# Kernel tuning notes

Hardware: AMD Instinct MI355X
Metric: run time of the kernel (lower is better)

## Reference

```python
import jax, jax.numpy as jnp
import numpy as np

N_NODES = 50000

def _sage(x, src, dst, Wl, bl, Wr):
    # PyG SAGEConv(aggr='mean'): out = lin_l(mean_{j in N(i)} x_j) + lin_r(x_i)
    msg = x[src]                                                    # [E, F] gather
    agg = jax.ops.segment_sum(msg, dst, num_segments=N_NODES)      # [N, F]
    cnt = jax.ops.segment_sum(jnp.ones((src.shape[0],), x.dtype), dst, num_segments=N_NODES)
    agg = agg / jnp.maximum(cnt, 1.0)[:, None]                     # mean aggregate
    return agg @ Wl + bl + x @ Wr                                   # lin_l has bias, lin_r does not


def setup_inputs() -> dict:
    key = jax.random.key(0)
    ks = jax.random.split(key, 14)
    d_in, d_h, d_out, n_edges = 128, 64, 4, 800000
    s = lambda k, shp, fan: jax.random.normal(k, shp, jnp.float32) * (1.0 / np.sqrt(fan))
    return {
        'x': jax.random.normal(ks[0], (N_NODES, d_in), jnp.float32),
        'edge_index': jax.random.randint(ks[1], (2, n_edges), 0, N_NODES, jnp.int64),
        'Wl1': s(ks[2], (d_in, d_h), d_in), 'bl1': jnp.zeros((d_h,), jnp.float32),
        'Wr1': s(ks[3], (d_in, d_h), d_in),
        'Wl2': s(ks[4], (d_h, d_h), d_h), 'bl2': jnp.zeros((d_h,), jnp.float32),
        'Wr2': s(ks[5], (d_h, d_h), d_h),
        'Wl3': s(ks[6], (d_h, d_h), d_h), 'bl3': jnp.zeros((d_h,), jnp.float32),
        'Wr3': s(ks[7], (d_h, d_h), d_h),
        'Wp': s(ks[8], (2 * d_h, d_out), 2 * d_h), 'bp': jnp.zeros((d_out,), jnp.float32),
    }


def reference(x, edge_index, Wl1, bl1, Wr1, Wl2, bl2, Wr2, Wl3, bl3, Wr3, Wp, bp):
    src, dst = edge_index[0], edge_index[1]
    # dropout is identity in eval mode
    h = jax.nn.elu(_sage(x, src, dst, Wl1, bl1, Wr1))
    h = jax.nn.elu(_sage(h, src, dst, Wl2, bl2, Wr2))
    h = jax.nn.elu(_sage(h, src, dst, Wl3, bl3, Wr3))
    edge_feat = jnp.concatenate([h[src], h[dst]], axis=1)  # [E, 2*hidden]
    return edge_feat @ Wp + bp                              # [E, output_dim]
```

## Files before the change

kernel.cpp:

```cpp
#include <hip/hip_runtime.h>
#include <hip/hip_bf16.h>

#define N_NODES 50000
#define N_EDGES 800000
#define D_IN 128
#define D_H 64
#define SCAN_BLOCKS 196
#define HIST_BLOCKS 3125
#define LIN1_BLOCKS 782
#define GL_BLOCKS 3125
#define ZROW 65535

#define F1L 0
#define F1R 8192
#define F2L 16384
#define F2R 20480
#define F3L 24576
#define F3R 28672
#define FRAG_TOTAL 32768

typedef short bf16x8 __attribute__((ext_vector_type(8)));
typedef float f32x4 __attribute__((ext_vector_type(4)));

__device__ __forceinline__ ushort f2bf(float f) {
    __hip_bfloat16 b = __float2bfloat16(f);
    return *reinterpret_cast<ushort*>(&b);
}
__device__ __forceinline__ float bf16_lo(unsigned int u) { return __uint_as_float(u << 16); }
__device__ __forceinline__ float bf16_hi(unsigned int u) { return __uint_as_float(u & 0xffff0000u); }

__device__ __forceinline__ void build_frag_one(const float* __restrict__ W, int local,
                                               ushort* __restrict__ frag, int fid) {
    int lane = local & 63;
    int ktnt = local >> 6;
    int kt = ktnt >> 2, nt = ktnt & 3;
    int quad = lane >> 4, col = lane & 15;
    ushort t0 = f2bf(W[(kt * 32 + quad * 8 + 0) * D_H + nt * 16 + col]);
    ushort t1 = f2bf(W[(kt * 32 + quad * 8 + 1) * D_H + nt * 16 + col]);
    ushort t2 = f2bf(W[(kt * 32 + quad * 8 + 2) * D_H + nt * 16 + col]);
    ushort t3 = f2bf(W[(kt * 32 + quad * 8 + 3) * D_H + nt * 16 + col]);
    ushort t4 = f2bf(W[(kt * 32 + quad * 8 + 4) * D_H + nt * 16 + col]);
    ushort t5 = f2bf(W[(kt * 32 + quad * 8 + 5) * D_H + nt * 16 + col]);
    ushort t6 = f2bf(W[(kt * 32 + quad * 8 + 6) * D_H + nt * 16 + col]);
    ushort t7 = f2bf(W[(kt * 32 + quad * 8 + 7) * D_H + nt * 16 + col]);
    uint4 v;
    v.x = (unsigned int)t0 | ((unsigned int)t1 << 16);
    v.y = (unsigned int)t2 | ((unsigned int)t3 << 16);
    v.z = (unsigned int)t4 | ((unsigned int)t5 << 16);
    v.w = (unsigned int)t6 | ((unsigned int)t7 << 16);
    *reinterpret_cast<uint4*>(frag + (size_t)fid * 8) = v;
}

__global__ void hist_frags_kernel(const int* __restrict__ dstv, int* __restrict__ cnt,
                                  ushort* __restrict__ rank,
                                  const float* __restrict__ Wl1, const float* __restrict__ Wr1,
                                  const float* __restrict__ Wl2, const float* __restrict__ Wr2,
                                  const float* __restrict__ Wl3, const float* __restrict__ Wr3,
                                  ushort* __restrict__ frag,
                                  ushort* __restrict__ Y1, ushort* __restrict__ Y2) {
    if (blockIdx.x < HIST_BLOCKS) {
        int e = blockIdx.x * 256 + threadIdx.x;
        if (e < N_EDGES) {
            int r = atomicAdd(&cnt[dstv[e]], 1);
            rank[e] = (ushort)r;
        }
    } else if (blockIdx.x < HIST_BLOCKS + 16) {
        int fid = (blockIdx.x - HIST_BLOCKS) * 256 + threadIdx.x;
        const float* W; int base;
        if (fid < 1024)      { W = Wl1; base = 0; }
        else if (fid < 2048) { W = Wr1; base = 1024; }
        else if (fid < 2560) { W = Wl2; base = 2048; }
        else if (fid < 3072) { W = Wr2; base = 2560; }
        else if (fid < 3584) { W = Wl3; base = 3072; }
        else                 { W = Wr3; base = 3584; }
        build_frag_one(W, fid - base, frag, fid);
    } else {
        int t = threadIdx.x;
        if (t < 64)       Y1[(size_t)ZROW * D_H + t] = 0;
        else if (t < 128) Y2[(size_t)ZROW * D_H + (t - 64)] = 0;
    }
}

__global__ void scan_partial(const int* __restrict__ cnt, int* __restrict__ blockSums) {
    __shared__ int s[256];
    int i = blockIdx.x * 256 + threadIdx.x;
    s[threadIdx.x] = (i < N_NODES) ? cnt[i] : 0;
    __syncthreads();
    for (int off = 128; off > 0; off >>= 1) {
        if (threadIdx.x < off) s[threadIdx.x] += s[threadIdx.x + off];
        __syncthreads();
    }
    if (threadIdx.x == 0) blockSums[blockIdx.x] = s[0];
}

__global__ void scan_final(const int* __restrict__ cnt, const int* __restrict__ blockSums,
                           int* __restrict__ row_ptr) {
    __shared__ int s[256];
    __shared__ int bs[256];
    int t = threadIdx.x;
    bs[t] = (t < SCAN_BLOCKS) ? blockSums[t] : 0;
    int i = blockIdx.x * 256 + t;
    s[t] = (i < N_NODES) ? cnt[i] : 0;
    __syncthreads();
    for (int off = 1; off < 256; off <<= 1) {
        int tmp1 = (t >= off) ? s[t - off] : 0;
        int tmp2 = (t >= off) ? bs[t - off] : 0;
        __syncthreads();
        s[t] += tmp1;
        bs[t] += tmp2;
        __syncthreads();
    }
    int blockExcl = (blockIdx.x > 0) ? bs[blockIdx.x - 1] : 0;
    int excl = blockExcl + ((t > 0) ? s[t - 1] : 0);
    if (i < N_NODES) row_ptr[i] = excl;
    if (i == 0) row_ptr[N_NODES] = N_EDGES;
}

__device__ __forceinline__ void lin1_body(int gwave, int lane, const float* __restrict__ hin,
                                          const ushort* __restrict__ fragWl,
                                          const ushort* __restrict__ fragWr,
                                          ushort* __restrict__ Y, ushort* __restrict__ Zb) {
    constexpr int KT = D_IN / 32;
    int m0 = gwave * 16;
    if (m0 >= N_NODES) return;
    int col = lane & 15;
    int quad = lane >> 4;

    bf16x8 blf2[KT][4], brf[KT][4];
#pragma unroll
    for (int kt = 0; kt < KT; ++kt)
#pragma unroll
        for (int nt = 0; nt < 4; ++nt) {
            size_t off = (size_t)((kt * 4 + nt) * 64 + lane) * 8;
            blf2[kt][nt] = __builtin_bit_cast(bf16x8, *reinterpret_cast<const uint4*>(fragWl + off));
            brf[kt][nt] = __builtin_bit_cast(bf16x8, *reinterpret_cast<const uint4*>(fragWr + off));
        }

    f32x4 accl0 = {0.f,0.f,0.f,0.f}, accl1 = accl0, accl2 = accl0, accl3 = accl0;
    f32x4 accr0 = accl0, accr1 = accl0, accr2 = accl0, accr3 = accl0;
    const float* arow = hin + (size_t)(m0 + col) * D_IN + quad * 8;
#pragma unroll
    for (int kt = 0; kt < KT; ++kt) {
        float4 a_lo = *reinterpret_cast<const float4*>(arow + kt * 32);
        float4 a_hi = *reinterpret_cast<const float4*>(arow + kt * 32 + 4);
        bf16x8 a;
        a[0] = (short)f2bf(a_lo.x); a[1] = (short)f2bf(a_lo.y);
        a[2] = (short)f2bf(a_lo.z); a[3] = (short)f2bf(a_lo.w);
        a[4] = (short)f2bf(a_hi.x); a[5] = (short)f2bf(a_hi.y);
        a[6] = (short)f2bf(a_hi.z); a[7] = (short)f2bf(a_hi.w);
        accl0 = __builtin_amdgcn_mfma_f32_16x16x32_bf16(a, blf2[kt][0], accl0, 0, 0, 0);
        accl1 = __builtin_amdgcn_mfma_f32_16x16x32_bf16(a, blf2[kt][1], accl1, 0, 0, 0);
        accl2 = __builtin_amdgcn_mfma_f32_16x16x32_bf16(a, blf2[kt][2], accl2, 0, 0, 0);
        accl3 = __builtin_amdgcn_mfma_f32_16x16x32_bf16(a, blf2[kt][3], accl3, 0, 0, 0);
        accr0 = __builtin_amdgcn_mfma_f32_16x16x32_bf16(a, brf[kt][0], accr0, 0, 0, 0);
        accr1 = __builtin_amdgcn_mfma_f32_16x16x32_bf16(a, brf[kt][1], accr1, 0, 0, 0);
        accr2 = __builtin_amdgcn_mfma_f32_16x16x32_bf16(a, brf[kt][2], accr2, 0, 0, 0);
        accr3 = __builtin_amdgcn_mfma_f32_16x16x32_bf16(a, brf[kt][3], accr3, 0, 0, 0);
    }
#pragma unroll
    for (int reg = 0; reg < 4; ++reg) {
        size_t r = (size_t)(m0 + quad * 4 + reg) * D_H;
        ushort* yp = Y + r;
        yp[0 * 16 + col] = f2bf(accl0[reg]);
        yp[1 * 16 + col] = f2bf(accl1[reg]);
        yp[2 * 16 + col] = f2bf(accl2[reg]);
        yp[3 * 16 + col] = f2bf(accl3[reg]);
        ushort* zp = Zb + r;
        zp[0 * 16 + col] = f2bf(accr0[reg]);
        zp[1 * 16 + col] = f2bf(accr1[reg]);
        zp[2 * 16 + col] = f2bf(accr2[reg]);
        zp[3 * 16 + col] = f2bf(accr3[reg]);
    }
}

__global__ void lin1_fill_kernel(const float* __restrict__ x, const ushort* __restrict__ wfrag,
                                 const int* __restrict__ srcv, const int* __restrict__ dstv,
                                 const ushort* __restrict__ rank, const int* __restrict__ row_ptr,
                                 ushort* __restrict__ csr_src,
                                 ushort* __restrict__ Y, ushort* __restrict__ Zb) {
    if (blockIdx.x < LIN1_BLOCKS) {
        int gwave = (blockIdx.x * 256 + threadIdx.x) >> 6;
        lin1_body(gwave, threadIdx.x & 63, x, wfrag + F1L, wfrag + F1R, Y, Zb);
    } else {
        int e = (blockIdx.x - LIN1_BLOCKS) * 256 + threadIdx.x;
        if (e < N_EDGES) {
            int d = dstv[e];
            int pos = row_ptr[d] + (int)rank[e];
            csr_src[pos] = (ushort)srcv[e];
        }
    }
}

template <bool FUSE_PROJ>
__global__ void gather_lin_kernel(const ushort* __restrict__ Y, const ushort* __restrict__ Zb,
                                  const float* __restrict__ bl,
                                  const int* __restrict__ row_ptr, const ushort* __restrict__ csr_src,
                                  const ushort* __restrict__ fragWl, const ushort* __restrict__ fragWr,
                                  ushort* __restrict__ Ynext, ushort* __restrict__ Zbnext,
                                  const float* __restrict__ Wp,
                                  float* __restrict__ ps, float* __restrict__ pd) {
    __shared__ ushort Hs[16][72];
    int w = threadIdx.x >> 6;
    int lane = threadIdx.x & 63;
    int wv = (blockIdx.x << 2) + w;
    int n0 = wv << 2;
    int g = lane >> 4;
    int l = lane & 15;

    int rp[5];
#pragma unroll
    for (int i = 0; i < 5; ++i) rp[i] = row_ptr[n0 + i];
    int deg[4];
#pragma unroll
    for (int n = 0; n < 4; ++n) deg[n] = rp[n + 1] - rp[n];
    int maxdeg = deg[0];
#pragma unroll
    for (int n = 1; n < 4; ++n) maxdeg = deg[n] > maxdeg ? deg[n] : maxdeg;

    float acc[4][4] = {{0.f}};
    const uint2* __restrict__ Y2 = reinterpret_cast<const uint2*>(Y);

    for (int base = 0; base < maxdeg; base += 64) {
        int idxv[4];
#pragma unroll
        for (int n = 0; n < 4; ++n) {
            int t = (int)csr_src[rp[n] + base + lane];
            idxv[n] = (base + lane < deg[n]) ? t : ZROW;
        }
        int kmax = maxdeg - base; if (kmax > 64) kmax = 64;
        for (int k = 0; k < kmax; k += 16) {
            uint2 rr[4][4];
#pragma unroll
            for (int n = 0; n < 4; ++n)
#pragma unroll
                for (int j = 0; j < 4; ++j) {
                    int s = __shfl(idxv[n], k + 4 * j + g);
                    rr[n][j] = Y2[s * 16 + l];
                }
#pragma unroll
            for (int n = 0; n < 4; ++n)
#pragma unroll
                for (int j = 0; j < 4; ++j) {
                    acc[n][0] += bf16_lo(rr[n][j].x); acc[n][1] += bf16_hi(rr[n][j].x);
                    acc[n][2] += bf16_lo(rr[n][j].y); acc[n][3] += bf16_hi(rr[n][j].y);
                }
        }
    }

#pragma unroll
    for (int n = 0; n < 4; ++n)
#pragma unroll
        for (int f = 0; f < 4; ++f) {
            acc[n][f] += __shfl_xor(acc[n][f], 16);
            acc[n][f] += __shfl_xor(acc[n][f], 32);
        }

    int node = n0 + g;
    float dgf = (g == 0) ? (float)deg[0] : (g == 1) ? (float)deg[1]
              : (g == 2) ? (float)deg[2] : (float)deg[3];
    float c0 = (g == 0) ? acc[0][0] : (g == 1) ? acc[1][0] : (g == 2) ? acc[2][0] : acc[3][0];
    float c1 = (g == 0) ? acc[0][1] : (g == 1) ? acc[1][1] : (g == 2) ? acc[2][1] : acc[3][1];
    float c2 = (g == 0) ? acc[0][2] : (g == 1) ? acc[1][2] : (g == 2) ? acc[2][2] : acc[3][2];
    float c3 = (g == 0) ? acc[0][3] : (g == 1) ? acc[1][3] : (g == 2) ? acc[2][3] : acc[3][3];
    float inv = 1.0f / fmaxf(dgf, 1.0f);
    float4 bv = reinterpret_cast<const float4*>(bl)[l];
    uint2 zr = reinterpret_cast<const uint2*>(Zb)[node * 16 + l];
    float v0 = c0 * inv + bv.x + bf16_lo(zr.x);
    float v1 = c1 * inv + bv.y + bf16_hi(zr.x);
    float v2 = c2 * inv + bv.z + bf16_lo(zr.y);
    float v3 = c3 * inv + bv.w + bf16_hi(zr.y);
    float o0 = v0 > 0.f ? v0 : expm1f(v0);
    float o1 = v1 > 0.f ? v1 : expm1f(v1);
    float o2 = v2 > 0.f ? v2 : expm1f(v2);
    float o3 = v3 > 0.f ? v3 : expm1f(v3);

    if constexpr (FUSE_PROJ) {
        float p0 = 0.f, p1 = 0.f, p2 = 0.f, p3 = 0.f;
        float q0 = 0.f, q1 = 0.f, q2 = 0.f, q3 = 0.f;
        float ov[4] = {o0, o1, o2, o3};
#pragma unroll
        for (int j = 0; j < 4; ++j) {
            int k = 4 * l + j;
            float4 wt = reinterpret_cast<const float4*>(Wp)[k];
            float4 wb = reinterpret_cast<const float4*>(Wp)[D_H + k];
            p0 += ov[j] * wt.x; p1 += ov[j] * wt.y; p2 += ov[j] * wt.z; p3 += ov[j] * wt.w;
            q0 += ov[j] * wb.x; q1 += ov[j] * wb.y; q2 += ov[j] * wb.z; q3 += ov[j] * wb.w;
        }
#pragma unroll
        for (int off = 1; off < 16; off <<= 1) {
            p0 += __shfl_xor(p0, off); p1 += __shfl_xor(p1, off);
            p2 += __shfl_xor(p2, off); p3 += __shfl_xor(p3, off);
            q0 += __shfl_xor(q0, off); q1 += __shfl_xor(q1, off);
            q2 += __shfl_xor(q2, off); q3 += __shfl_xor(q3, off);
        }
        if (l == 0) {
            float4 pv; pv.x = p0; pv.y = p1; pv.z = p2; pv.w = p3;
            float4 qv; qv.x = q0; qv.y = q1; qv.z = q2; qv.w = q3;
            reinterpret_cast<float4*>(ps)[node] = pv;
            reinterpret_cast<float4*>(pd)[node] = qv;
        }
    } else {
        ushort4 ob;
        ob.x = f2bf(o0); ob.y = f2bf(o1); ob.z = f2bf(o2); ob.w = f2bf(o3);
        int localrow = w * 4 + g;
        *reinterpret_cast<ushort4*>(&Hs[localrow][4 * l]) = ob;
        __syncthreads();

        int col = lane & 15;
        int quad = lane >> 4;
        bf16x8 blf0 = __builtin_bit_cast(bf16x8,
            *reinterpret_cast<const uint4*>(fragWl + (size_t)((0 * 4 + w) * 64 + lane) * 8));
        bf16x8 blf1 = __builtin_bit_cast(bf16x8,
            *reinterpret_cast<const uint4*>(fragWl + (size_t)((1 * 4 + w) * 64 + lane) * 8));
        bf16x8 brf0 = __builtin_bit_cast(bf16x8,
            *reinterpret_cast<const uint4*>(fragWr + (size_t)((0 * 4 + w) * 64 + lane) * 8));
        bf16x8 brf1 = __builtin_bit_cast(bf16x8,
            *reinterpret_cast<const uint4*>(fragWr + (size_t)((1 * 4 + w) * 64 + lane) * 8));
        bf16x8 a0 = __builtin_bit_cast(bf16x8,
            *reinterpret_cast<const uint4*>(&Hs[col][quad * 8]));
        bf16x8 a1 = __builtin_bit_cast(bf16x8,
            *reinterpret_cast<const uint4*>(&Hs[col][32 + quad * 8]));
        f32x4 accl = {0.f,0.f,0.f,0.f};
        f32x4 accr = {0.f,0.f,0.f,0.f};
        accl = __builtin_amdgcn_mfma_f32_16x16x32_bf16(a0, blf0, accl, 0, 0, 0);
        accl = __builtin_amdgcn_mfma_f32_16x16x32_bf16(a1, blf1, accl, 0, 0, 0);
        accr = __builtin_amdgcn_mfma_f32_16x16x32_bf16(a0, brf0, accr, 0, 0, 0);
        accr = __builtin_amdgcn_mfma_f32_16x16x32_bf16(a1, brf1, accr, 0, 0, 0);

        int n0base = blockIdx.x * 16;
#pragma unroll
        for (int reg = 0; reg < 4; ++reg) {
            size_t r = (size_t)(n0base + quad * 4 + reg) * D_H + w * 16 + col;
            Ynext[r]  = f2bf(accl[reg]);
            Zbnext[r] = f2bf(accr[reg]);
        }
    }
}

__global__ void edge_final_kernel(const int* __restrict__ srcv, const int* __restrict__ dstv,
                                  const float* __restrict__ ps, const float* __restrict__ pd,
                                  const float* __restrict__ bp, float* __restrict__ out) {
    int e = blockIdx.x * 256 + threadIdx.x;
    const int HALF = N_EDGES / 2;
    if (e >= HALF) return;
    int e2 = e + HALF;
    int s0 = srcv[e], d0 = dstv[e];
    int s1 = srcv[e2], d1 = dstv[e2];
    float4 a0 = reinterpret_cast<const float4*>(ps)[s0];
    float4 b0 = reinterpret_cast<const float4*>(pd)[d0];
    float4 a1 = reinterpret_cast<const float4*>(ps)[s1];
    float4 b1 = reinterpret_cast<const float4*>(pd)[d1];
    float bx = bp[0], by = bp[1], bz = bp[2], bw = bp[3];
    float4 o0, o1;
    o0.x = a0.x + b0.x + bx; o0.y = a0.y + b0.y + by;
    o0.z = a0.z + b0.z + bz; o0.w = a0.w + b0.w + bw;
    o1.x = a1.x + b1.x + bx; o1.y = a1.y + b1.y + by;
    o1.z = a1.z + b1.z + bz; o1.w = a1.w + b1.w + bw;
    reinterpret_cast<float4*>(out)[e] = o0;
    reinterpret_cast<float4*>(out)[e2] = o1;
}

extern "C" void kernel_launch(void* const* d_in, const int* in_sizes, int n_in,
                              void* d_out, int out_size, void* d_ws, size_t ws_size,
                              hipStream_t stream) {
    const float* x   = (const float*)d_in[0];
    const int*   ei  = (const int*)d_in[1];
    const float* Wl1 = (const float*)d_in[2];
    const float* bl1 = (const float*)d_in[3];
    const float* Wr1 = (const float*)d_in[4];
    const float* Wl2 = (const float*)d_in[5];
    const float* bl2 = (const float*)d_in[6];
    const float* Wr2 = (const float*)d_in[7];
    const float* Wl3 = (const float*)d_in[8];
    const float* bl3 = (const float*)d_in[9];
    const float* Wr3 = (const float*)d_in[10];
    const float* Wp  = (const float*)d_in[11];
    const float* bp  = (const float*)d_in[12];
    float* out = (float*)d_out;

    const int* srcv = ei;
    const int* dstv = ei + N_EDGES;

    int*   cnt       = (int*)d_ws;
    int*   blockSums = cnt + 50000;
    int*   row_ptr   = blockSums + 256;
    ushort* rank     = (ushort*)(row_ptr + 50001);
    ushort* csr_src  = rank + 800000;
    ushort* wfrag = (ushort*)(((uintptr_t)(csr_src + 800000 + 4096) + 127) & ~(uintptr_t)127);
    ushort* Y1  = (ushort*)(((uintptr_t)(wfrag + FRAG_TOTAL) + 127) & ~(uintptr_t)127);
    ushort* Y2  = Y1 + (size_t)65536 * D_H;
    ushort* Zb1 = Y2 + (size_t)65536 * D_H;
    ushort* Zb2 = Zb1 + (size_t)N_NODES * D_H;
    float* ps = (float*)(((uintptr_t)(Zb2 + (size_t)N_NODES * D_H) + 15) & ~(uintptr_t)15);
    float* pd = ps + (size_t)N_NODES * 4;

    hipMemsetAsync(cnt, 0, N_NODES * sizeof(int), stream);
    hist_frags_kernel<<<HIST_BLOCKS + 17, 256, 0, stream>>>(dstv, cnt, rank, Wl1, Wr1, Wl2, Wr2,
                                                            Wl3, Wr3, wfrag, Y1, Y2);
    scan_partial<<<SCAN_BLOCKS, 256, 0, stream>>>(cnt, blockSums);
    scan_final<<<SCAN_BLOCKS, 256, 0, stream>>>(cnt, blockSums, row_ptr);

    lin1_fill_kernel<<<LIN1_BLOCKS + HIST_BLOCKS, 256, 0, stream>>>(x, wfrag, srcv, dstv,
                                                                    rank, row_ptr, csr_src,
                                                                    Y1, Zb1);

    gather_lin_kernel<false><<<GL_BLOCKS, 256, 0, stream>>>(Y1, Zb1, bl1, row_ptr, csr_src,
                                                            wfrag + F2L, wfrag + F2R, Y2, Zb2,
                                                            nullptr, nullptr, nullptr);

    gather_lin_kernel<false><<<GL_BLOCKS, 256, 0, stream>>>(Y2, Zb2, bl2, row_ptr, csr_src,
                                                            wfrag + F3L, wfrag + F3R, Y1, Zb1,
                                                            nullptr, nullptr, nullptr);

    gather_lin_kernel<true><<<GL_BLOCKS, 256, 0, stream>>>(Y1, Zb1, bl3, row_ptr, csr_src,
                                                           nullptr, nullptr, nullptr, nullptr,
                                                           Wp, ps, pd);

    edge_final_kernel<<<(N_EDGES / 2 + 255) / 256, 256, 0, stream>>>(srcv, dstv, ps, pd, bp, out);
}
```

Measured before the change: 235.6 us.

## Sort nodes by degree into bins so gather waves get balanced neighbor counts

Builds a 64-bin degree histogram during the scan and a counting-sort permutation of nodes by degree. The gather/linear kernels then process nodes in permuted order, so the four nodes sharing a wave have similar degrees and less lane time is wasted waiting on the maximum degree. Output rows are scattered through a shared-memory node-id table. The edge output kernel also now handles four edges per thread instead of two. The cost is extra atomics, a perm array, and scattered row writes that lose contiguity.

```diff
diff --git a/kernel.cpp b/kernel.cpp
--- a/kernel.cpp
+++ b/kernel.cpp
@@ -8,8 +8,10 @@
 #define SCAN_BLOCKS 196
 #define HIST_BLOCKS 3125
 #define LIN1_BLOCKS 782
+#define PERM_BLOCKS 196
 #define GL_BLOCKS 3125
 #define ZROW 65535
+#define DBINS 64
 
 #define F1L 0
 #define F1R 8192
@@ -81,20 +83,28 @@
     }
 }
 
-__global__ void scan_partial(const int* __restrict__ cnt, int* __restrict__ blockSums) {
+__global__ void scan_partial(const int* __restrict__ cnt, int* __restrict__ blockSums,
+                             int* __restrict__ dhist) {
     __shared__ int s[256];
-    int i = blockIdx.x * 256 + threadIdx.x;
-    s[threadIdx.x] = (i < N_NODES) ? cnt[i] : 0;
+    __shared__ int ldh[DBINS];
+    int t = threadIdx.x;
+    if (t < DBINS) ldh[t] = 0;
+    int i = blockIdx.x * 256 + t;
+    int myc = (i < N_NODES) ? cnt[i] : 0;
+    s[t] = myc;
     __syncthreads();
+    if (i < N_NODES) atomicAdd(&ldh[myc < DBINS ? myc : DBINS - 1], 1);
     for (int off = 128; off > 0; off >>= 1) {
-        if (threadIdx.x < off) s[threadIdx.x] += s[threadIdx.x + off];
+        if (t < off) s[t] += s[t + off];
         __syncthreads();
     }
-    if (threadIdx.x == 0) blockSums[blockIdx.x] = s[0];
+    if (t == 0) blockSums[blockIdx.x] = s[0];
+    if (t < DBINS && ldh[t] > 0) atomicAdd(&dhist[t], ldh[t]);
 }
 
 __global__ void scan_final(const int* __restrict__ cnt, const int* __restrict__ blockSums,
-                           int* __restrict__ row_ptr) {
+                           int* __restrict__ row_ptr,
+                           const int* __restrict__ dhist, int* __restrict__ dcur) {
     __shared__ int s[256];
     __shared__ int bs[256];
     int t = threadIdx.x;
@@ -114,6 +124,17 @@
     int excl = blockExcl + ((t > 0) ? s[t - 1] : 0);
     if (i < N_NODES) row_ptr[i] = excl;
     if (i == 0) row_ptr[N_NODES] = N_EDGES;
+
+    if (blockIdx.x == 0 && t < DBINS) {
+        int c = dhist[t];
+        int v = c;
+#pragma unroll
+        for (int off = 1; off < DBINS; off <<= 1) {
+            int u = __shfl_up(v, off);
+            if (t >= off) v += u;
+        }
+        dcur[t] = v - c;
+    }
 }
 
 __device__ __forceinline__ void lin1_body(int gwave, int lane, const float* __restrict__ hin,
@@ -177,17 +198,27 @@
                                  const int* __restrict__ srcv, const int* __restrict__ dstv,
                                  const ushort* __restrict__ rank, const int* __restrict__ row_ptr,
                                  ushort* __restrict__ csr_src,
+                                 const int* __restrict__ cnt, int* __restrict__ dcur,
+                                 int* __restrict__ perm,
                                  ushort* __restrict__ Y, ushort* __restrict__ Zb) {
     if (blockIdx.x < LIN1_BLOCKS) {
         int gwave = (blockIdx.x * 256 + threadIdx.x) >> 6;
         lin1_body(gwave, threadIdx.x & 63, x, wfrag + F1L, wfrag + F1R, Y, Zb);
-    } else {
+    } else if (blockIdx.x < LIN1_BLOCKS + HIST_BLOCKS) {
         int e = (blockIdx.x - LIN1_BLOCKS) * 256 + threadIdx.x;
         if (e < N_EDGES) {
             int d = dstv[e];
             int pos = row_ptr[d] + (int)rank[e];
             csr_src[pos] = (ushort)srcv[e];
         }
+    } else {
+        int i = (blockIdx.x - LIN1_BLOCKS - HIST_BLOCKS) * 256 + threadIdx.x;
+        if (i < N_NODES) {
+            int deg = cnt[i];
+            int bin = deg < DBINS ? deg : DBINS - 1;
+            int pos = atomicAdd(&dcur[bin], 1);
+            perm[pos] = i;
+        }
     }
 }
 
@@ -195,24 +226,26 @@
 __global__ void gather_lin_kernel(const ushort* __restrict__ Y, const ushort* __restrict__ Zb,
                                   const float* __restrict__ bl,
                                   const int* __restrict__ row_ptr, const ushort* __restrict__ csr_src,
+                                  const int* __restrict__ perm,
                                   const ushort* __restrict__ fragWl, const ushort* __restrict__ fragWr,
                                   ushort* __restrict__ Ynext, ushort* __restrict__ Zbnext,
                                   const float* __restrict__ Wp,
                                   float* __restrict__ ps, float* __restrict__ pd) {
     __shared__ ushort Hs[16][72];
+    __shared__ int nid[16];
     int w = threadIdx.x >> 6;
     int lane = threadIdx.x & 63;
-    int wv = (blockIdx.x << 2) + w;
-    int n0 = wv << 2;
     int g = lane >> 4;
     int l = lane & 15;
-
-    int rp[5];
-#pragma unroll
-    for (int i = 0; i < 5; ++i) rp[i] = row_ptr[n0 + i];
-    int deg[4];
-#pragma unroll
-    for (int n = 0; n < 4; ++n) deg[n] = rp[n + 1] - rp[n];
+    int base16 = blockIdx.x * 16;
+
+    int nd[4], rpl[4], deg[4];
+#pragma unroll
+    for (int n = 0; n < 4; ++n) {
+        nd[n] = perm[base16 + w * 4 + n];
+        rpl[n] = row_ptr[nd[n]];
+        deg[n] = row_ptr[nd[n] + 1] - rpl[n];
+    }
     int maxdeg = deg[0];
 #pragma unroll
     for (int n = 1; n < 4; ++n) maxdeg = deg[n] > maxdeg ? deg[n] : maxdeg;
@@ -224,7 +257,7 @@
         int idxv[4];
 #pragma unroll
         for (int n = 0; n < 4; ++n) {
-            int t = (int)csr_src[rp[n] + base + lane];
+            int t = (int)csr_src[rpl[n] + base + lane];
             idxv[n] = (base + lane < deg[n]) ? t : ZROW;
         }
         int kmax = maxdeg - base; if (kmax > 64) kmax = 64;
@@ -255,7 +288,7 @@
             acc[n][f] += __shfl_xor(acc[n][f], 32);
         }
 
-    int node = n0 + g;
+    int node = (g == 0) ? nd[0] : (g == 1) ? nd[1] : (g == 2) ? nd[2] : nd[3];
     float dgf = (g == 0) ? (float)deg[0] : (g == 1) ? (float)deg[1]
               : (g == 2) ? (float)deg[2] : (float)deg[3];
     float c0 = (g == 0) ? acc[0][0] : (g == 1) ? acc[1][0] : (g == 2) ? acc[2][0] : acc[3][0];
@@ -303,6 +336,7 @@
         ushort4 ob;
         ob.x = f2bf(o0); ob.y = f2bf(o1); ob.z = f2bf(o2); ob.w = f2bf(o3);
         int localrow = w * 4 + g;
+        if (l == 0) nid[localrow] = node;
         *reinterpret_cast<ushort4*>(&Hs[localrow][4 * l]) = ob;
         __syncthreads();
 
@@ -327,10 +361,10 @@
         accr = __builtin_amdgcn_mfma_f32_16x16x32_bf16(a0, brf0, accr, 0, 0, 0);
         accr = __builtin_amdgcn_mfma_f32_16x16x32_bf16(a1, brf1, accr, 0, 0, 0);
 
-        int n0base = blockIdx.x * 16;
 #pragma unroll
         for (int reg = 0; reg < 4; ++reg) {
-            size_t r = (size_t)(n0base + quad * 4 + reg) * D_H + w * 16 + col;
+            int trow = nid[quad * 4 + reg];
+            size_t r = (size_t)trow * D_H + w * 16 + col;
             Ynext[r]  = f2bf(accl[reg]);
             Zbnext[r] = f2bf(accr[reg]);
         }
@@ -341,23 +375,19 @@
                                   const float* __restrict__ ps, const float* __restrict__ pd,
                                   const float* __restrict__ bp, float* __restrict__ out) {
     int e = blockIdx.x * 256 + threadIdx.x;
-    const int HALF = N_EDGES / 2;
-    if (e >= HALF) return;
-    int e2 = e + HALF;
-    int s0 = srcv[e], d0 = dstv[e];
-    int s1 = srcv[e2], d1 = dstv[e2];
-    float4 a0 = reinterpret_cast<const float4*>(ps)[s0];
-    float4 b0 = reinterpret_cast<const float4*>(pd)[d0];
-    float4 a1 = reinterpret_cast<const float4*>(ps)[s1];
-    float4 b1 = reinterpret_cast<const float4*>(pd)[d1];
+    const int Q = N_EDGES / 4;
+    if (e >= Q) return;
     float bx = bp[0], by = bp[1], bz = bp[2], bw = bp[3];
-    float4 o0, o1;
-    o0.x = a0.x + b0.x + bx; o0.y = a0.y + b0.y + by;
-    o0.z = a0.z + b0.z + bz; o0.w = a0.w + b0.w + bw;
-    o1.x = a1.x + b1.x + bx; o1.y = a1.y + b1.y + by;
-    o1.z = a1.z + b1.z + bz; o1.w = a1.w + b1.w + bw;
-    reinterpret_cast<float4*>(out)[e] = o0;
-    reinterpret_cast<float4*>(out)[e2] = o1;
+#pragma unroll
+    for (int h = 0; h < 4; ++h) {
+        int ee = e + h * Q;
+        float4 a = reinterpret_cast<const float4*>(ps)[srcv[ee]];
+        float4 b = reinterpret_cast<const float4*>(pd)[dstv[ee]];
+        float4 o;
+        o.x = a.x + b.x + bx; o.y = a.y + b.y + by;
+        o.z = a.z + b.z + bz; o.w = a.w + b.w + bw;
+        reinterpret_cast<float4*>(out)[ee] = o;
+    }
 }
 
 extern "C" void kernel_launch(void* const* d_in, const int* in_sizes, int n_in,
@@ -382,9 +412,12 @@
     const int* dstv = ei + N_EDGES;
 
     int*   cnt       = (int*)d_ws;
-    int*   blockSums = cnt + 50000;
+    int*   dhist     = cnt + 50000;
+    int*   dcur      = dhist + 64;
+    int*   blockSums = dcur + 64;
     int*   row_ptr   = blockSums + 256;
-    ushort* rank     = (ushort*)(row_ptr + 50001);
+    int*   perm      = row_ptr + 50001;
+    ushort* rank     = (ushort*)(perm + 50000);
     ushort* csr_src  = rank + 800000;
     ushort* wfrag = (ushort*)(((uintptr_t)(csr_src + 800000 + 4096) + 127) & ~(uintptr_t)127);
     ushort* Y1  = (ushort*)(((uintptr_t)(wfrag + FRAG_TOTAL) + 127) & ~(uintptr_t)127);
@@ -394,27 +427,26 @@
     float* ps = (float*)(((uintptr_t)(Zb2 + (size_t)N_NODES * D_H) + 15) & ~(uintptr_t)15);
     float* pd = ps + (size_t)N_NODES * 4;
 
-    hipMemsetAsync(cnt, 0, N_NODES * sizeof(int), stream);
+    hipMemsetAsync(cnt, 0, (50000 + 64) * sizeof(int), stream);
     hist_frags_kernel<<<HIST_BLOCKS + 17, 256, 0, stream>>>(dstv, cnt, rank, Wl1, Wr1, Wl2, Wr2,
                                                             Wl3, Wr3, wfrag, Y1, Y2);
-    scan_partial<<<SCAN_BLOCKS, 256, 0, stream>>>(cnt, blockSums);
-    scan_final<<<SCAN_BLOCKS, 256, 0, stream>>>(cnt, blockSums, row_ptr);
-
-    lin1_fill_kernel<<<LIN1_BLOCKS + HIST_BLOCKS, 256, 0, stream>>>(x, wfrag, srcv, dstv,
-                                                                    rank, row_ptr, csr_src,
-                                                                    Y1, Zb1);
-
-    gather_lin_kernel<false><<<GL_BLOCKS, 256, 0, stream>>>(Y1, Zb1, bl1, row_ptr, csr_src,
+    scan_partial<<<SCAN_BLOCKS, 256, 0, stream>>>(cnt, blockSums, dhist);
+    scan_final<<<SCAN_BLOCKS, 256, 0, stream>>>(cnt, blockSums, row_ptr, dhist, dcur);
+
+    lin1_fill_kernel<<<LIN1_BLOCKS + HIST_BLOCKS + PERM_BLOCKS, 256, 0, stream>>>(
+        x, wfrag, srcv, dstv, rank, row_ptr, csr_src, cnt, dcur, perm, Y1, Zb1);
+
+    gather_lin_kernel<false><<<GL_BLOCKS, 256, 0, stream>>>(Y1, Zb1, bl1, row_ptr, csr_src, perm,
                                                             wfrag + F2L, wfrag + F2R, Y2, Zb2,
                                                             nullptr, nullptr, nullptr);
 
-    gather_lin_kernel<false><<<GL_BLOCKS, 256, 0, stream>>>(Y2, Zb2, bl2, row_ptr, csr_src,
+    gather_lin_kernel<false><<<GL_BLOCKS, 256, 0, stream>>>(Y2, Zb2, bl2, row_ptr, csr_src, perm,
                                                             wfrag + F3L, wfrag + F3R, Y1, Zb1,
                                                             nullptr, nullptr, nullptr);
 
-    gather_lin_kernel<true><<<GL_BLOCKS, 256, 0, stream>>>(Y1, Zb1, bl3, row_ptr, csr_src,
+    gather_lin_kernel<true><<<GL_BLOCKS, 256, 0, stream>>>(Y1, Zb1, bl3, row_ptr, csr_src, perm,
                                                            nullptr, nullptr, nullptr, nullptr,
                                                            Wp, ps, pd);
 
-    edge_final_kernel<<<(N_EDGES / 2 + 255) / 256, 256, 0, stream>>>(srcv, dstv, ps, pd, bp, out);
-}
+    edge_final_kernel<<<(N_EDGES / 4 + 255) / 256, 256, 0, stream>>>(srcv, dstv, ps, pd, bp, out);
+}
```

New measurement: 340.8 us. +44.6%, slower.
